# Performance work log

Hardware: AMD Instinct MI355X
Metric: run time of the kernel (lower is better)

Reference implementation:

```python
import jax, jax.numpy as jnp
import numpy as np

N, E, D, H, B = 10000, 160000, 128, 1, 4
SLOPE = 0.01  # negative_slope from DeepQNet default


def gat_layer(x, node_state, src, dst, W, att_src, att_dst, Wns, bns, bias):
    # x: [N,D] or [B,N,D]; node_state: [B,N,1]
    xs = x + node_state @ Wns + bns              # [B,N,D]
    Bx, Nn = xs.shape[0], xs.shape[1]
    h = (xs @ W).reshape(Bx, Nn, H, D)           # [B,N,H,C]
    a_src = (h * att_src).sum(-1)                # [B,N,H]
    a_dst = (h * att_dst).sum(-1)                # [B,N,H]
    ae = a_src[:, src] + a_dst[:, dst]           # [B,Etot,H]
    ae = jnp.where(ae > 0, ae, SLOPE * ae)       # leaky_relu
    ae_t = jnp.moveaxis(ae, 1, 0)                # [Etot,B,H]
    m = jax.ops.segment_max(ae_t, dst, num_segments=Nn)   # [N,B,H]
    e = jnp.exp(ae_t - m[dst])
    s = jax.ops.segment_sum(e, dst, num_segments=Nn)
    alpha = e / s[dst]                           # [Etot,B,H]
    h_e = jnp.moveaxis(h, 1, 0)                  # [N,B,H,C]
    msg = alpha[..., None] * h_e[src]            # [Etot,B,H,C]
    out = jax.ops.segment_sum(msg, dst, num_segments=Nn)  # [N,B,H,C]
    out = jnp.moveaxis(out, 0, 1).mean(2) + bias # concat=False -> head mean
    return jax.nn.relu(out)


def setup_inputs() -> dict:
    key = jax.random.key(0)
    ks = jax.random.split(key, 16)
    edges = jax.random.randint(ks[0], (2, E), 0, N)
    loop = jnp.arange(N)
    edge_index = jnp.concatenate([edges, jnp.stack([loop, loop])], axis=1)  # add_self_loops
    state = jax.random.uniform(ks[1], (B, N), dtype=jnp.float32)
    strucEmb = jax.random.normal(ks[2], (N, D), dtype=jnp.float32) * 0.1
    s = 0.05
    return {
        "state": state,
        "strucEmb": strucEmb,
        "edge_index": edge_index,
        "gat_W": jax.random.normal(ks[3], (3, D, H * D), dtype=jnp.float32) * s,
        "gat_att_src": jax.random.normal(ks[4], (3, H, D), dtype=jnp.float32) * s,
        "gat_att_dst": jax.random.normal(ks[5], (3, H, D), dtype=jnp.float32) * s,
        "gat_Wns": jax.random.normal(ks[6], (3, 1, D), dtype=jnp.float32) * s,
        "gat_bns": jnp.zeros((3, D), jnp.float32),
        "gat_bias": jnp.zeros((3, D), jnp.float32),
        "W1": jax.random.normal(ks[7], (D, D), dtype=jnp.float32) * s,
        "b1": jnp.zeros((D,), jnp.float32),
        "W2": jax.random.normal(ks[8], (D, D), dtype=jnp.float32) * s,
        "b2": jnp.zeros((D,), jnp.float32),
        "W3": jax.random.normal(ks[9], (2 * D, 1), dtype=jnp.float32) * s,
        "b3": jnp.zeros((1,), jnp.float32),
    }


def reference(state, strucEmb, edge_index, gat_W, gat_att_src, gat_att_dst,
              gat_Wns, gat_bns, gat_bias, W1, b1, W2, b2, W3, b3):
    src, dst = edge_index[0], edge_index[1]
    rs = state.reshape(state.shape[0], N, 1)     # [B,N,1]
    x = strucEmb
    for l in range(3):
        x = gat_layer(x, rs, src, dst, gat_W[l], gat_att_src[l], gat_att_dst[l],
                      gat_Wns[l], gat_bns[l], gat_bias[l])
    state_emb = x.sum(1)                         # [B,D]
    beta_state = state_emb @ W1 + b1             # [B,D]
    beta_action = x @ W2 + b2                    # [B,N,D]  (is_for_learn=True path)
    expand_state = jnp.broadcast_to(beta_state[:, None, :], beta_action.shape)
    out = jax.nn.relu(jnp.concatenate([expand_state, beta_action], axis=2))
    return out @ W3 + b3                         # [B,N,1]
```

## Files before the change

kernel.cpp:

```cpp
#include <hip/hip_runtime.h>
#include <math.h>

#define N_NODES 10000
#define B_SZ 4
#define SLOPE 0.01f
#define BN (B_SZ * N_NODES)
#define PADK 136

typedef __attribute__((ext_vector_type(8))) short short8;
typedef __attribute__((ext_vector_type(4))) float float4v;

__device__ __forceinline__ unsigned short f2bf(float f) {
    unsigned u = __builtin_bit_cast(unsigned, f);
    u += 0x7fffu + ((u >> 16) & 1u);
    return (unsigned short)(u >> 16);
}
__device__ __forceinline__ float bf2f(unsigned short s) {
    unsigned u = ((unsigned)s) << 16;
    return __builtin_bit_cast(float, u);
}
__device__ __forceinline__ float bflo(unsigned u) { return __builtin_bit_cast(float, u << 16); }
__device__ __forceinline__ float bfhi(unsigned u) { return __builtin_bit_cast(float, u & 0xffff0000u); }



__global__ __launch_bounds__(256) void setup_kernel(
    const float* __restrict__ strucEmb, const float* __restrict__ state,
    const float* __restrict__ Wns0, const float* __restrict__ bns0,
    const float* __restrict__ gatW, const float* __restrict__ W2,
    unsigned short* __restrict__ XS,
    unsigned short* __restrict__ whi, unsigned short* __restrict__ wlo,
    int* deg, int* cursor, float* state_emb)
{
    int bx = blockIdx.x, tid = threadIdx.x;
    if (bx < 2500) {
        int base = (bx * 256 + tid) * 8;
        int g = base >> 7, d0 = base & 127;
        int n = g - (g / N_NODES) * N_NODES;
        float st = state[g];
        const float* se = strucEmb + (size_t)n * 128 + d0;
        const float* wp = Wns0 + d0;
        const float* bp = bns0 + d0;
        short8 v;
#pragma unroll
        for (int j = 0; j < 8; j++)
            v[j] = (short)f2bf(se[j] + st * wp[j] + bp[j]);
        *(short8*)(XS + base) = v;
    } else if (bx < 2756) {
        int i = (bx - 2500) * 256 + tid;
        int w = i >> 14, rem = i & 16383;
        int k = rem >> 7, c = rem & 127;
        const float* src = (w < 3) ? (gatW + (size_t)w * 16384) : W2;
        float v = src[k * 128 + c];
        unsigned short h = f2bf(v);
        whi[w * 16384 + c * 128 + k] = h;
        wlo[w * 16384 + c * 128 + k] = f2bf(v - bf2f(h));
    } else {
        int i = (bx - 2756) * 256 + tid;
        if (i < N_NODES) { deg[i] = 0; cursor[i] = 0; }
        if (i < 512) state_emb[i] = 0.f;
    }
}


__global__ __launch_bounds__(256) void hist_kernel(const int* __restrict__ dst, int Etot, int* deg) {
    int e = blockIdx.x * 256 + threadIdx.x;
    if (e < Etot) atomicAdd(&deg[dst[e]], 1);
}

__global__ __launch_bounds__(1024) void scan_kernel(const int* __restrict__ deg, int* __restrict__ rowOff) {
    __shared__ int wsum[16];
    int tid = threadIdx.x;
    int lane = tid & 63, wid = tid >> 6;
    int base = tid * 10;
    int v[10]; int tot = 0;
#pragma unroll
    for (int j = 0; j < 10; j++) {
        int idx = base + j;
        int d = (idx < N_NODES) ? deg[idx] : 0;
        tot += d; v[j] = tot;
    }
    int incl = tot;
    for (int off = 1; off < 64; off <<= 1) {
        int t = __shfl_up(incl, off, 64);
        if (lane >= off) incl += t;
    }
    if (lane == 63) wsum[wid] = incl;
    __syncthreads();
    if (wid == 0) {
        int wv = (lane < 16) ? wsum[lane] : 0;
        for (int off = 1; off < 16; off <<= 1) {
            int t = __shfl_up(wv, off, 64);
            if (lane >= off) wv += t;
        }
        if (lane < 16) wsum[lane] = wv;
    }
    __syncthreads();
    int waveoff = (wid > 0) ? wsum[wid - 1] : 0;
    int excl = waveoff + incl - tot;
    if (tid == 0) rowOff[0] = 0;
#pragma unroll
    for (int j = 0; j < 10; j++) {
        int idx = base + j;
        if (idx < N_NODES) rowOff[idx + 1] = excl + v[j];
    }
}

__global__ __launch_bounds__(256) void scatter_kernel(const int* __restrict__ src, const int* __restrict__ dst,
                                                      int Etot, const int* __restrict__ rowOff,
                                                      int* cursor, int* __restrict__ srcLst) {
    int e = blockIdx.x * 256 + threadIdx.x;
    if (e < Etot) {
        int d = dst[e];
        int pos = rowOff[d] + atomicAdd(&cursor[d], 1);
        srcLst[pos] = src[e];
    }
}


__global__ __launch_bounds__(256) void gemm_att_mfma(
    const unsigned short* __restrict__ XS,
    const unsigned short* __restrict__ WThi, const unsigned short* __restrict__ WTlo,
    const float* __restrict__ attS, const float* __restrict__ attD,
    unsigned short* __restrict__ Hout, float* __restrict__ aSrcP, float* __restrict__ aDstP)
{
    __shared__ __align__(16) unsigned short sCus[64 * PADK];
    __shared__ float sAs[128], sAd[128];
    __shared__ float sPart[64 * 8];

    int tid = threadIdx.x;
    int g0 = blockIdx.x * 64;
    int w = tid >> 6, lane = tid & 63;
    int quad = lane >> 4, mcol = lane & 15;

    if (tid < 128) { sAs[tid] = attS[tid]; sAd[tid] = attD[tid]; }

    float4v acc[4][2];
#pragma unroll
    for (int mt = 0; mt < 4; mt++)
#pragma unroll
        for (int nt = 0; nt < 2; nt++) acc[mt][nt] = (float4v){0.f, 0.f, 0.f, 0.f};

#pragma unroll 1
    for (int term = 0; term < 2; term++) {
        const unsigned short* WT = term ? WTlo : WThi;
        short8 Bf[4][2];
#pragma unroll
        for (int kc = 0; kc < 4; kc++)
#pragma unroll
            for (int nt = 0; nt < 2; nt++)
                Bf[kc][nt] = *(const short8*)(WT + (w * 32 + nt * 16 + mcol) * 128 + kc * 32 + quad * 8);
#pragma unroll
        for (int kc = 0; kc < 4; kc++) {
            short8 Aa[4];
#pragma unroll
            for (int mt = 0; mt < 4; mt++)
                Aa[mt] = *(const short8*)(XS + (size_t)(g0 + mt * 16 + mcol) * 128 + kc * 32 + quad * 8);
#pragma unroll
            for (int mt = 0; mt < 4; mt++)
#pragma unroll
                for (int nt = 0; nt < 2; nt++)
                    acc[mt][nt] = __builtin_amdgcn_mfma_f32_16x16x32_bf16(Aa[mt], Bf[kc][nt], acc[mt][nt], 0, 0, 0);
        }
    }

    __syncthreads();

    float pp[16], pd[16];
#pragma unroll
    for (int r16 = 0; r16 < 16; r16++) { pp[r16] = 0.f; pd[r16] = 0.f; }
#pragma unroll
    for (int mt = 0; mt < 4; mt++)
#pragma unroll
        for (int nt = 0; nt < 2; nt++)
#pragma unroll
            for (int reg = 0; reg < 4; reg++) {
                int row = mt * 16 + quad * 4 + reg;
                int col = w * 32 + nt * 16 + mcol;
                float v = acc[mt][nt][reg];
                sCus[row * PADK + col] = f2bf(v);
                pp[mt * 4 + reg] += v * sAs[col];
                pd[mt * 4 + reg] += v * sAd[col];
            }
#pragma unroll
    for (int off = 1; off < 16; off <<= 1)
#pragma unroll
        for (int r16 = 0; r16 < 16; r16++) {
            pp[r16] += __shfl_xor(pp[r16], off);
            pd[r16] += __shfl_xor(pd[r16], off);
        }
    if (mcol == 0) {
#pragma unroll
        for (int r16 = 0; r16 < 16; r16++) {
            int row = (r16 >> 2) * 16 + quad * 4 + (r16 & 3);
            sPart[row * 8 + w * 2 + 0] = pp[r16];
            sPart[row * 8 + w * 2 + 1] = pd[r16];
        }
    }
    __syncthreads();

    for (int i = tid; i < 64 * 16; i += 256) {
        int r = i >> 4, c8 = i & 15;
        uint4 u = *(uint4*)(sCus + r * PADK + c8 * 8);
        *(uint4*)(Hout + (size_t)(g0 + r) * 128 + c8 * 8) = u;
    }
    if (tid < 64) {
        float s0 = sPart[tid * 8] + sPart[tid * 8 + 2] + sPart[tid * 8 + 4] + sPart[tid * 8 + 6];
        float s1 = sPart[tid * 8 + 1] + sPart[tid * 8 + 3] + sPart[tid * 8 + 5] + sPart[tid * 8 + 7];
        aSrcP[g0 + tid] = s0;
        aDstP[g0 + tid] = s1;
    }
}


__global__ __launch_bounds__(256) void sm_agg_kernel(
    const int* __restrict__ rowOff, const int* __restrict__ srcLst,
    const float* __restrict__ aSrcP, const float* __restrict__ aDstP,
    const unsigned short* __restrict__ H,
    const float* __restrict__ bias,
    const float* __restrict__ state, const float* __restrict__ wnsN,
    const float* __restrict__ bnsN, int addNext,
    unsigned short* __restrict__ Xout)
{
    __shared__ int   sSrcB[4 * 64];
    __shared__ float sAeB[4 * 64];
    int tid = threadIdx.x;
    int w = tid >> 6, t = tid & 63;
    int blk = blockIdx.x;
    int xcd = blk & 7;
    int b = xcd >> 1;
    int n = (((xcd & 1) * (N_NODES / 8) + (blk >> 3)) << 2) + w;
    int gb = b * N_NODES;
    int start = rowOff[n], end = rowOff[n + 1];
    int cnt = end - start;
    float adst = aDstP[gb + n];
    int*   sSrc = sSrcB + w * 64;
    float* sAe  = sAeB + w * 64;
    const uint4* H4 = (const uint4*)H;

    if (cnt <= 64) {
        float ae = -1e30f;
        if (t < cnt) {
            int sn = srcLst[start + t];
            sSrc[t] = sn;
            float v = aSrcP[gb + sn] + adst;
            ae = v > 0.f ? v : SLOPE * v;
        }
        float m = ae;
        m = fmaxf(m, __shfl_xor(m, 1));  m = fmaxf(m, __shfl_xor(m, 2));
        m = fmaxf(m, __shfl_xor(m, 4));  m = fmaxf(m, __shfl_xor(m, 8));
        m = fmaxf(m, __shfl_xor(m, 16)); m = fmaxf(m, __shfl_xor(m, 32));
        float e = (t < cnt) ? __expf(ae - m) : 0.f;
        float s = e;
        s += __shfl_xor(s, 1);  s += __shfl_xor(s, 2);  s += __shfl_xor(s, 4);
        s += __shfl_xor(s, 8);  s += __shfl_xor(s, 16); s += __shfl_xor(s, 32);
        float inv = 1.f / s;
        if (t < cnt) sAe[t] = e * inv;
        int cntE = (cnt + 3) & ~3;
        if (t >= cnt && t < cntE) { sSrc[t] = n; sAe[t] = 0.f; }

        int esub = t >> 4, c16 = t & 15;
        float a0 = 0.f, a1 = 0.f, a2 = 0.f, a3 = 0.f, a4 = 0.f, a5 = 0.f, a6 = 0.f, a7 = 0.f;
        int j = 0;
        for (; j + 16 <= cntE; j += 16) {
            uint4 h[4]; float al[4];
#pragma unroll
            for (int r = 0; r < 4; r++) {
                int jj = j + r * 4 + esub;
                h[r] = H4[(size_t)(gb + sSrc[jj]) * 16 + c16];
                al[r] = sAe[jj];
            }
#pragma unroll
            for (int r = 0; r < 4; r++) {
                a0 += al[r] * bflo(h[r].x); a1 += al[r] * bfhi(h[r].x);
                a2 += al[r] * bflo(h[r].y); a3 += al[r] * bfhi(h[r].y);
                a4 += al[r] * bflo(h[r].z); a5 += al[r] * bfhi(h[r].z);
                a6 += al[r] * bflo(h[r].w); a7 += al[r] * bfhi(h[r].w);
            }
        }
        for (; j < cntE; j += 4) {
            int jj = j + esub;
            uint4 hv = H4[(size_t)(gb + sSrc[jj]) * 16 + c16];
            float al = sAe[jj];
            a0 += al * bflo(hv.x); a1 += al * bfhi(hv.x);
            a2 += al * bflo(hv.y); a3 += al * bfhi(hv.y);
            a4 += al * bflo(hv.z); a5 += al * bfhi(hv.z);
            a6 += al * bflo(hv.w); a7 += al * bfhi(hv.w);
        }
        a0 += __shfl_xor(a0, 16); a1 += __shfl_xor(a1, 16);
        a2 += __shfl_xor(a2, 16); a3 += __shfl_xor(a3, 16);
        a4 += __shfl_xor(a4, 16); a5 += __shfl_xor(a5, 16);
        a6 += __shfl_xor(a6, 16); a7 += __shfl_xor(a7, 16);
        a0 += __shfl_xor(a0, 32); a1 += __shfl_xor(a1, 32);
        a2 += __shfl_xor(a2, 32); a3 += __shfl_xor(a3, 32);
        a4 += __shfl_xor(a4, 32); a5 += __shfl_xor(a5, 32);
        a6 += __shfl_xor(a6, 32); a7 += __shfl_xor(a7, 32);
        if (esub == 0) {
            int d0 = c16 * 8;
            float o0 = fmaxf(a0 + bias[d0],     0.f);
            float o1 = fmaxf(a1 + bias[d0 + 1], 0.f);
            float o2 = fmaxf(a2 + bias[d0 + 2], 0.f);
            float o3 = fmaxf(a3 + bias[d0 + 3], 0.f);
            float o4 = fmaxf(a4 + bias[d0 + 4], 0.f);
            float o5 = fmaxf(a5 + bias[d0 + 5], 0.f);
            float o6 = fmaxf(a6 + bias[d0 + 6], 0.f);
            float o7 = fmaxf(a7 + bias[d0 + 7], 0.f);
            if (addNext) {
                float st = state[gb + n];
                o0 += st * wnsN[d0]     + bnsN[d0];
                o1 += st * wnsN[d0 + 1] + bnsN[d0 + 1];
                o2 += st * wnsN[d0 + 2] + bnsN[d0 + 2];
                o3 += st * wnsN[d0 + 3] + bnsN[d0 + 3];
                o4 += st * wnsN[d0 + 4] + bnsN[d0 + 4];
                o5 += st * wnsN[d0 + 5] + bnsN[d0 + 5];
                o6 += st * wnsN[d0 + 6] + bnsN[d0 + 6];
                o7 += st * wnsN[d0 + 7] + bnsN[d0 + 7];
            }
            uint4 u;
            u.x = (unsigned)f2bf(o0) | ((unsigned)f2bf(o1) << 16);
            u.y = (unsigned)f2bf(o2) | ((unsigned)f2bf(o3) << 16);
            u.z = (unsigned)f2bf(o4) | ((unsigned)f2bf(o5) << 16);
            u.w = (unsigned)f2bf(o6) | ((unsigned)f2bf(o7) << 16);
            ((uint4*)Xout)[(size_t)(gb + n) * 16 + c16] = u;
        }
    } else {
        const unsigned* Hu = (const unsigned*)H;
        float m = -1e30f;
        for (int i = start + t; i < end; i += 64) {
            int sn = srcLst[i];
            float v = aSrcP[gb + sn] + adst;
            m = fmaxf(m, v > 0.f ? v : SLOPE * v);
        }
        m = fmaxf(m, __shfl_xor(m, 1));  m = fmaxf(m, __shfl_xor(m, 2));
        m = fmaxf(m, __shfl_xor(m, 4));  m = fmaxf(m, __shfl_xor(m, 8));
        m = fmaxf(m, __shfl_xor(m, 16)); m = fmaxf(m, __shfl_xor(m, 32));
        float s = 0.f;
        for (int i = start + t; i < end; i += 64) {
            int sn = srcLst[i];
            float v = aSrcP[gb + sn] + adst;
            float ae2 = v > 0.f ? v : SLOPE * v;
            s += __expf(ae2 - m);
        }
        s += __shfl_xor(s, 1);  s += __shfl_xor(s, 2);  s += __shfl_xor(s, 4);
        s += __shfl_xor(s, 8);  s += __shfl_xor(s, 16); s += __shfl_xor(s, 32);
        float inv = 1.f / s;
        float accx = 0.f, accy = 0.f;
        for (int c0 = start; c0 < end; c0 += 64) {
            int c = min(64, end - c0);
            if (t < c) {
                int sn = srcLst[c0 + t];
                sSrc[t] = sn;
                float v = aSrcP[gb + sn] + adst;
                float ae2 = v > 0.f ? v : SLOPE * v;
                sAe[t] = __expf(ae2 - m);
            }
            for (int j = 0; j < c; j++) {
                float a0 = sAe[j];
                unsigned h0 = Hu[(size_t)(gb + sSrc[j]) * 64 + t];
                accx += a0 * bflo(h0);
                accy += a0 * bfhi(h0);
            }
        }
        float ox = fmaxf(accx * inv + bias[2 * t], 0.f);
        float oy = fmaxf(accy * inv + bias[2 * t + 1], 0.f);
        if (addNext) {
            float st = state[gb + n];
            ox += st * wnsN[2 * t]     + bnsN[2 * t];
            oy += st * wnsN[2 * t + 1] + bnsN[2 * t + 1];
        }
        ((unsigned*)Xout)[(size_t)(gb + n) * 64 + t] =
            (unsigned)f2bf(ox) | ((unsigned)f2bf(oy) << 16);
    }
}


__global__ __launch_bounds__(128) void sum_nodes_kernel(const unsigned short* __restrict__ X, float* state_emb) {
    int cx = blockIdx.x, b = blockIdx.y, d = threadIdx.x;
    int n0 = cx * 157, n1 = n0 + 157;
    if (n1 > N_NODES) n1 = N_NODES;
    float acc = 0.f;
    for (int n = n0; n < n1; n++) acc += bf2f(X[(size_t)(b * N_NODES + n) * 128 + d]);
    atomicAdd(&state_emb[b * 128 + d], acc);
}


__global__ __launch_bounds__(256) void final_mfma(
    const unsigned short* __restrict__ X,
    const unsigned short* __restrict__ WThi, const unsigned short* __restrict__ WTlo,
    const float* __restrict__ b2, const float* __restrict__ W3,
    const float* __restrict__ b3,
    const float* __restrict__ state_emb, const float* __restrict__ W1,
    const float* __restrict__ b1,
    float* __restrict__ out)
{
    __shared__ float sB2[128], sW3[128];
    __shared__ float sPart[64 * 4];
    __shared__ float sC1p[8], sC1[4];

    int tid = threadIdx.x;
    int g0 = blockIdx.x * 64;
    int w = tid >> 6, lane = tid & 63;
    int quad = lane >> 4, mcol = lane & 15;

    if (tid < 128) { sB2[tid] = b2[tid]; sW3[tid] = W3[128 + tid]; }

    {
        int d = tid & 127;
        int bh = tid >> 7;
        float p0 = b1[d], p1 = b1[d];
        for (int k = 0; k < 128; k++) {
            float wv = W1[k * 128 + d];
            p0 += state_emb[bh * 128 + k] * wv;
            p1 += state_emb[(bh + 2) * 128 + k] * wv;
        }
        float w3d = W3[d];
        p0 = fmaxf(p0, 0.f) * w3d;
        p1 = fmaxf(p1, 0.f) * w3d;
#pragma unroll
        for (int off = 1; off < 64; off <<= 1) {
            p0 += __shfl_xor(p0, off);
            p1 += __shfl_xor(p1, off);
        }
        if (lane == 0) { sC1p[w * 2 + 0] = p0; sC1p[w * 2 + 1] = p1; }
    }
    __syncthreads();
    if (tid == 0) {
        sC1[0] = sC1p[0] + sC1p[2];  sC1[2] = sC1p[1] + sC1p[3];
        sC1[1] = sC1p[4] + sC1p[6];  sC1[3] = sC1p[5] + sC1p[7];
    }

    float4v acc[4][2];
#pragma unroll
    for (int mt = 0; mt < 4; mt++)
#pragma unroll
        for (int nt = 0; nt < 2; nt++) acc[mt][nt] = (float4v){0.f, 0.f, 0.f, 0.f};

#pragma unroll 1
    for (int term = 0; term < 2; term++) {
        const unsigned short* WT = term ? WTlo : WThi;
        short8 Bf[4][2];
#pragma unroll
        for (int kc = 0; kc < 4; kc++)
#pragma unroll
            for (int nt = 0; nt < 2; nt++)
                Bf[kc][nt] = *(const short8*)(WT + (w * 32 + nt * 16 + mcol) * 128 + kc * 32 + quad * 8);
#pragma unroll
        for (int kc = 0; kc < 4; kc++) {
            short8 Aa[4];
#pragma unroll
            for (int mt = 0; mt < 4; mt++)
                Aa[mt] = *(const short8*)(X + (size_t)(g0 + mt * 16 + mcol) * 128 + kc * 32 + quad * 8);
#pragma unroll
            for (int mt = 0; mt < 4; mt++)
#pragma unroll
                for (int nt = 0; nt < 2; nt++)
                    acc[mt][nt] = __builtin_amdgcn_mfma_f32_16x16x32_bf16(Aa[mt], Bf[kc][nt], acc[mt][nt], 0, 0, 0);
        }
    }

    float pp[16];
#pragma unroll
    for (int r16 = 0; r16 < 16; r16++) pp[r16] = 0.f;
#pragma unroll
    for (int mt = 0; mt < 4; mt++)
#pragma unroll
        for (int nt = 0; nt < 2; nt++)
#pragma unroll
            for (int reg = 0; reg < 4; reg++) {
                int col = w * 32 + nt * 16 + mcol;
                float v = acc[mt][nt][reg] + sB2[col];
                v = v > 0.f ? v : 0.f;
                pp[mt * 4 + reg] += v * sW3[col];
            }
#pragma unroll
    for (int off = 1; off < 16; off <<= 1)
#pragma unroll
        for (int r16 = 0; r16 < 16; r16++)
            pp[r16] += __shfl_xor(pp[r16], off);
    if (mcol == 0) {
#pragma unroll
        for (int r16 = 0; r16 < 16; r16++) {
            int row = (r16 >> 2) * 16 + quad * 4 + (r16 & 3);
            sPart[row * 4 + w] = pp[r16];
        }
    }
    __syncthreads();
    if (tid < 64) {
        float p = sPart[tid * 4] + sPart[tid * 4 + 1] + sPart[tid * 4 + 2] + sPart[tid * 4 + 3];
        int g = g0 + tid;
        int b = g / N_NODES;
        out[g] = p + sC1[b] + b3[0];
    }
}


extern "C" void kernel_launch(void* const* d_in, const int* in_sizes, int n_in,
                              void* d_out, int out_size, void* d_ws, size_t ws_size,
                              hipStream_t stream) {
    const float* state    = (const float*)d_in[0];
    const float* strucEmb = (const float*)d_in[1];
    const int*   edge_idx = (const int*)d_in[2];
    const float* gat_W    = (const float*)d_in[3];
    const float* gat_aS   = (const float*)d_in[4];
    const float* gat_aD   = (const float*)d_in[5];
    const float* gat_Wns  = (const float*)d_in[6];
    const float* gat_bns  = (const float*)d_in[7];
    const float* gat_bias = (const float*)d_in[8];
    const float* W1 = (const float*)d_in[9];
    const float* b1 = (const float*)d_in[10];
    const float* W2 = (const float*)d_in[11];
    const float* b2 = (const float*)d_in[12];
    const float* W3 = (const float*)d_in[13];
    const float* b3 = (const float*)d_in[14];
    float* out = (float*)d_out;

    int Etot = in_sizes[2] / 2;
    const int* srcArr = edge_idx;
    const int* dstArr = edge_idx + Etot;

    float* ws = (float*)d_ws;
    unsigned short* Xb = (unsigned short*)ws;
    unsigned short* Hb = (unsigned short*)(ws + 2560000);
    float* aSrcP       = ws + 5120000;
    float* aDstP       = ws + 5160000;
    float* state_emb   = ws + 5200000;
    unsigned short* whi = (unsigned short*)(ws + 5200516);
    unsigned short* wlo = whi + 4 * 16384;
    int*   iws         = (int*)(ws + 5200516 + 65536);
    int*   rowOff      = iws;
    int*   deg         = iws + 10001;
    int*   cursor      = deg + 10000;
    int*   srcLst      = cursor + 10000;

    setup_kernel<<<2796, 256, 0, stream>>>(strucEmb, state, gat_Wns, gat_bns,
                                           gat_W, W2, Xb, whi, wlo, deg, cursor, state_emb);
    hist_kernel<<<(Etot + 255) / 256, 256, 0, stream>>>(dstArr, Etot, deg);
    scan_kernel<<<1, 1024, 0, stream>>>(deg, rowOff);
    scatter_kernel<<<(Etot + 255) / 256, 256, 0, stream>>>(srcArr, dstArr, Etot, rowOff, cursor, srcLst);

    for (int l = 0; l < 3; l++) {
        gemm_att_mfma<<<BN / 64, 256, 0, stream>>>(
            Xb, whi + (size_t)l * 16384, wlo + (size_t)l * 16384,
            gat_aS + l * 128, gat_aD + l * 128, Hb, aSrcP, aDstP);
        sm_agg_kernel<<<N_NODES, 256, 0, stream>>>(
            rowOff, srcLst, aSrcP, aDstP, Hb, gat_bias + l * 128,
            state, gat_Wns + (l + 1 < 3 ? (l + 1) * 128 : 0),
            gat_bns + (l + 1 < 3 ? (l + 1) * 128 : 0), (l < 2) ? 1 : 0, Xb);
    }

    sum_nodes_kernel<<<dim3(64, B_SZ), 128, 0, stream>>>(Xb, state_emb);
    final_mfma<<<BN / 64, 256, 0, stream>>>(Xb, whi + 3 * 16384, wlo + 3 * 16384,
                                            b2, W3, b3, state_emb, W1, b1, out);
}
```

Before: 323.4 us.

## Process all four batches per wavefront in softmax-aggregation kernel

Each wavefront now handles one destination node across all four batch entries instead of one (node, batch) pair. CSR row offsets, source indices and shared-memory staging are loaded once and reused for four batches, and four independent H gathers are issued per edge. The grid shrinks fourfold and the XCD-aware block remapping is dropped. In exchange register pressure rises (32 accumulators plus in-flight loads), which may lower occupancy.

```diff
diff --git a/kernel.cpp b/kernel.cpp
--- a/kernel.cpp
+++ b/kernel.cpp
@@ -223,153 +223,196 @@
     unsigned short* __restrict__ Xout)
 {
     __shared__ int   sSrcB[4 * 64];
-    __shared__ float sAeB[4 * 64];
+    __shared__ float sAeB[4 * 4 * 64];
     int tid = threadIdx.x;
     int w = tid >> 6, t = tid & 63;
-    int blk = blockIdx.x;
-    int xcd = blk & 7;
-    int b = xcd >> 1;
-    int n = (((xcd & 1) * (N_NODES / 8) + (blk >> 3)) << 2) + w;
-    int gb = b * N_NODES;
+    int n = blockIdx.x * 4 + w;
     int start = rowOff[n], end = rowOff[n + 1];
     int cnt = end - start;
-    float adst = aDstP[gb + n];
     int*   sSrc = sSrcB + w * 64;
-    float* sAe  = sAeB + w * 64;
+    float* sAe  = sAeB + w * 256;
     const uint4* H4 = (const uint4*)H;
 
+    float adstb[4];
+#pragma unroll
+    for (int b = 0; b < 4; b++) adstb[b] = aDstP[b * N_NODES + n];
+
     if (cnt <= 64) {
-        float ae = -1e30f;
+        int sn = n;
+        if (t < cnt) { sn = srcLst[start + t]; sSrc[t] = sn; }
+        float ae0 = -1e30f, ae1 = -1e30f, ae2 = -1e30f, ae3 = -1e30f;
+        {
+            float v0 = aSrcP[0 * N_NODES + sn] + adstb[0];
+            float v1 = aSrcP[1 * N_NODES + sn] + adstb[1];
+            float v2 = aSrcP[2 * N_NODES + sn] + adstb[2];
+            float v3 = aSrcP[3 * N_NODES + sn] + adstb[3];
+            if (t < cnt) {
+                ae0 = v0 > 0.f ? v0 : SLOPE * v0;
+                ae1 = v1 > 0.f ? v1 : SLOPE * v1;
+                ae2 = v2 > 0.f ? v2 : SLOPE * v2;
+                ae3 = v3 > 0.f ? v3 : SLOPE * v3;
+            }
+        }
+        float m0 = ae0, m1 = ae1, m2 = ae2, m3 = ae3;
+#pragma unroll
+        for (int off = 1; off < 64; off <<= 1) {
+            m0 = fmaxf(m0, __shfl_xor(m0, off));
+            m1 = fmaxf(m1, __shfl_xor(m1, off));
+            m2 = fmaxf(m2, __shfl_xor(m2, off));
+            m3 = fmaxf(m3, __shfl_xor(m3, off));
+        }
+        float e0 = (t < cnt) ? __expf(ae0 - m0) : 0.f;
+        float e1 = (t < cnt) ? __expf(ae1 - m1) : 0.f;
+        float e2 = (t < cnt) ? __expf(ae2 - m2) : 0.f;
+        float e3 = (t < cnt) ? __expf(ae3 - m3) : 0.f;
+        float s0 = e0, s1 = e1, s2 = e2, s3 = e3;
+#pragma unroll
+        for (int off = 1; off < 64; off <<= 1) {
+            s0 += __shfl_xor(s0, off);
+            s1 += __shfl_xor(s1, off);
+            s2 += __shfl_xor(s2, off);
+            s3 += __shfl_xor(s3, off);
+        }
         if (t < cnt) {
-            int sn = srcLst[start + t];
-            sSrc[t] = sn;
-            float v = aSrcP[gb + sn] + adst;
-            ae = v > 0.f ? v : SLOPE * v;
-        }
-        float m = ae;
-        m = fmaxf(m, __shfl_xor(m, 1));  m = fmaxf(m, __shfl_xor(m, 2));
-        m = fmaxf(m, __shfl_xor(m, 4));  m = fmaxf(m, __shfl_xor(m, 8));
-        m = fmaxf(m, __shfl_xor(m, 16)); m = fmaxf(m, __shfl_xor(m, 32));
-        float e = (t < cnt) ? __expf(ae - m) : 0.f;
-        float s = e;
-        s += __shfl_xor(s, 1);  s += __shfl_xor(s, 2);  s += __shfl_xor(s, 4);
-        s += __shfl_xor(s, 8);  s += __shfl_xor(s, 16); s += __shfl_xor(s, 32);
-        float inv = 1.f / s;
-        if (t < cnt) sAe[t] = e * inv;
+            sAe[0 * 64 + t] = e0 / s0;
+            sAe[1 * 64 + t] = e1 / s1;
+            sAe[2 * 64 + t] = e2 / s2;
+            sAe[3 * 64 + t] = e3 / s3;
+        }
         int cntE = (cnt + 3) & ~3;
-        if (t >= cnt && t < cntE) { sSrc[t] = n; sAe[t] = 0.f; }
+        if (t >= cnt && t < cntE) {
+            sSrc[t] = n;
+            sAe[0 * 64 + t] = 0.f; sAe[1 * 64 + t] = 0.f;
+            sAe[2 * 64 + t] = 0.f; sAe[3 * 64 + t] = 0.f;
+        }
 
         int esub = t >> 4, c16 = t & 15;
-        float a0 = 0.f, a1 = 0.f, a2 = 0.f, a3 = 0.f, a4 = 0.f, a5 = 0.f, a6 = 0.f, a7 = 0.f;
+        float a[4][8];
+#pragma unroll
+        for (int b = 0; b < 4; b++)
+#pragma unroll
+            for (int k = 0; k < 8; k++) a[b][k] = 0.f;
+
         int j = 0;
-        for (; j + 16 <= cntE; j += 16) {
-            uint4 h[4]; float al[4];
-#pragma unroll
-            for (int r = 0; r < 4; r++) {
-                int jj = j + r * 4 + esub;
-                h[r] = H4[(size_t)(gb + sSrc[jj]) * 16 + c16];
-                al[r] = sAe[jj];
-            }
-#pragma unroll
-            for (int r = 0; r < 4; r++) {
-                a0 += al[r] * bflo(h[r].x); a1 += al[r] * bfhi(h[r].x);
-                a2 += al[r] * bflo(h[r].y); a3 += al[r] * bfhi(h[r].y);
-                a4 += al[r] * bflo(h[r].z); a5 += al[r] * bfhi(h[r].z);
-                a6 += al[r] * bflo(h[r].w); a7 += al[r] * bfhi(h[r].w);
+        for (; j + 8 <= cntE; j += 8) {
+            int j0 = j + esub, j1 = j + 4 + esub;
+            int sn0 = sSrc[j0], sn1 = sSrc[j1];
+            uint4 h0[4], h1[4]; float l0[4], l1[4];
+#pragma unroll
+            for (int b = 0; b < 4; b++) {
+                h0[b] = H4[((size_t)(b * N_NODES + sn0)) * 16 + c16];
+                h1[b] = H4[((size_t)(b * N_NODES + sn1)) * 16 + c16];
+                l0[b] = sAe[b * 64 + j0];
+                l1[b] = sAe[b * 64 + j1];
+            }
+#pragma unroll
+            for (int b = 0; b < 4; b++) {
+                a[b][0] += l0[b] * bflo(h0[b].x); a[b][1] += l0[b] * bfhi(h0[b].x);
+                a[b][2] += l0[b] * bflo(h0[b].y); a[b][3] += l0[b] * bfhi(h0[b].y);
+                a[b][4] += l0[b] * bflo(h0[b].z); a[b][5] += l0[b] * bfhi(h0[b].z);
+                a[b][6] += l0[b] * bflo(h0[b].w); a[b][7] += l0[b] * bfhi(h0[b].w);
+                a[b][0] += l1[b] * bflo(h1[b].x); a[b][1] += l1[b] * bfhi(h1[b].x);
+                a[b][2] += l1[b] * bflo(h1[b].y); a[b][3] += l1[b] * bfhi(h1[b].y);
+                a[b][4] += l1[b] * bflo(h1[b].z); a[b][5] += l1[b] * bfhi(h1[b].z);
+                a[b][6] += l1[b] * bflo(h1[b].w); a[b][7] += l1[b] * bfhi(h1[b].w);
             }
         }
         for (; j < cntE; j += 4) {
             int jj = j + esub;
-            uint4 hv = H4[(size_t)(gb + sSrc[jj]) * 16 + c16];
-            float al = sAe[jj];
-            a0 += al * bflo(hv.x); a1 += al * bfhi(hv.x);
-            a2 += al * bflo(hv.y); a3 += al * bfhi(hv.y);
-            a4 += al * bflo(hv.z); a5 += al * bfhi(hv.z);
-            a6 += al * bflo(hv.w); a7 += al * bfhi(hv.w);
-        }
-        a0 += __shfl_xor(a0, 16); a1 += __shfl_xor(a1, 16);
-        a2 += __shfl_xor(a2, 16); a3 += __shfl_xor(a3, 16);
-        a4 += __shfl_xor(a4, 16); a5 += __shfl_xor(a5, 16);
-        a6 += __shfl_xor(a6, 16); a7 += __shfl_xor(a7, 16);
-        a0 += __shfl_xor(a0, 32); a1 += __shfl_xor(a1, 32);
-        a2 += __shfl_xor(a2, 32); a3 += __shfl_xor(a3, 32);
-        a4 += __shfl_xor(a4, 32); a5 += __shfl_xor(a5, 32);
-        a6 += __shfl_xor(a6, 32); a7 += __shfl_xor(a7, 32);
+            int sn2 = sSrc[jj];
+            uint4 h[4]; float al[4];
+#pragma unroll
+            for (int b = 0; b < 4; b++) {
+                h[b] = H4[((size_t)(b * N_NODES + sn2)) * 16 + c16];
+                al[b] = sAe[b * 64 + jj];
+            }
+#pragma unroll
+            for (int b = 0; b < 4; b++) {
+                a[b][0] += al[b] * bflo(h[b].x); a[b][1] += al[b] * bfhi(h[b].x);
+                a[b][2] += al[b] * bflo(h[b].y); a[b][3] += al[b] * bfhi(h[b].y);
+                a[b][4] += al[b] * bflo(h[b].z); a[b][5] += al[b] * bfhi(h[b].z);
+                a[b][6] += al[b] * bflo(h[b].w); a[b][7] += al[b] * bfhi(h[b].w);
+            }
+        }
+#pragma unroll
+        for (int b = 0; b < 4; b++)
+#pragma unroll
+            for (int k = 0; k < 8; k++) {
+                a[b][k] += __shfl_xor(a[b][k], 16);
+                a[b][k] += __shfl_xor(a[b][k], 32);
+            }
         if (esub == 0) {
             int d0 = c16 * 8;
-            float o0 = fmaxf(a0 + bias[d0],     0.f);
-            float o1 = fmaxf(a1 + bias[d0 + 1], 0.f);
-            float o2 = fmaxf(a2 + bias[d0 + 2], 0.f);
-            float o3 = fmaxf(a3 + bias[d0 + 3], 0.f);
-            float o4 = fmaxf(a4 + bias[d0 + 4], 0.f);
-            float o5 = fmaxf(a5 + bias[d0 + 5], 0.f);
-            float o6 = fmaxf(a6 + bias[d0 + 6], 0.f);
-            float o7 = fmaxf(a7 + bias[d0 + 7], 0.f);
+#pragma unroll
+            for (int b = 0; b < 4; b++) {
+                float o[8];
+#pragma unroll
+                for (int k = 0; k < 8; k++) o[k] = fmaxf(a[b][k] + bias[d0 + k], 0.f);
+                if (addNext) {
+                    float st = state[b * N_NODES + n];
+#pragma unroll
+                    for (int k = 0; k < 8; k++) o[k] += st * wnsN[d0 + k] + bnsN[d0 + k];
+                }
+                uint4 u;
+                u.x = (unsigned)f2bf(o[0]) | ((unsigned)f2bf(o[1]) << 16);
+                u.y = (unsigned)f2bf(o[2]) | ((unsigned)f2bf(o[3]) << 16);
+                u.z = (unsigned)f2bf(o[4]) | ((unsigned)f2bf(o[5]) << 16);
+                u.w = (unsigned)f2bf(o[6]) | ((unsigned)f2bf(o[7]) << 16);
+                ((uint4*)Xout)[((size_t)(b * N_NODES + n)) * 16 + c16] = u;
+            }
+        }
+    } else {
+        const unsigned* Hu = (const unsigned*)H;
+#pragma unroll 1
+        for (int bb = 0; bb < 4; bb++) {
+            int gb = bb * N_NODES;
+            float adst = adstb[bb];
+            float m = -1e30f;
+            for (int i = start + t; i < end; i += 64) {
+                int sn = srcLst[i];
+                float v = aSrcP[gb + sn] + adst;
+                m = fmaxf(m, v > 0.f ? v : SLOPE * v);
+            }
+            m = fmaxf(m, __shfl_xor(m, 1));  m = fmaxf(m, __shfl_xor(m, 2));
+            m = fmaxf(m, __shfl_xor(m, 4));  m = fmaxf(m, __shfl_xor(m, 8));
+            m = fmaxf(m, __shfl_xor(m, 16)); m = fmaxf(m, __shfl_xor(m, 32));
+            float s = 0.f;
+            for (int i = start + t; i < end; i += 64) {
+                int sn = srcLst[i];
+                float v = aSrcP[gb + sn] + adst;
+                float ae2 = v > 0.f ? v : SLOPE * v;
+                s += __expf(ae2 - m);
+            }
+            s += __shfl_xor(s, 1);  s += __shfl_xor(s, 2);  s += __shfl_xor(s, 4);
+            s += __shfl_xor(s, 8);  s += __shfl_xor(s, 16); s += __shfl_xor(s, 32);
+            float inv = 1.f / s;
+            float accx = 0.f, accy = 0.f;
+            for (int c0 = start; c0 < end; c0 += 64) {
+                int c = min(64, end - c0);
+                if (t < c) {
+                    int sn = srcLst[c0 + t];
+                    sSrc[t] = sn;
+                    float v = aSrcP[gb + sn] + adst;
+                    float ae2 = v > 0.f ? v : SLOPE * v;
+                    sAe[t] = __expf(ae2 - m);
+                }
+                for (int j = 0; j < c; j++) {
+                    float a0 = sAe[j];
+                    unsigned h0 = Hu[(size_t)(gb + sSrc[j]) * 64 + t];
+                    accx += a0 * bflo(h0);
+                    accy += a0 * bfhi(h0);
+                }
+            }
+            float ox = fmaxf(accx * inv + bias[2 * t], 0.f);
+            float oy = fmaxf(accy * inv + bias[2 * t + 1], 0.f);
             if (addNext) {
                 float st = state[gb + n];
-                o0 += st * wnsN[d0]     + bnsN[d0];
-                o1 += st * wnsN[d0 + 1] + bnsN[d0 + 1];
-                o2 += st * wnsN[d0 + 2] + bnsN[d0 + 2];
-                o3 += st * wnsN[d0 + 3] + bnsN[d0 + 3];
-                o4 += st * wnsN[d0 + 4] + bnsN[d0 + 4];
-                o5 += st * wnsN[d0 + 5] + bnsN[d0 + 5];
-                o6 += st * wnsN[d0 + 6] + bnsN[d0 + 6];
-                o7 += st * wnsN[d0 + 7] + bnsN[d0 + 7];
-            }
-            uint4 u;
-            u.x = (unsigned)f2bf(o0) | ((unsigned)f2bf(o1) << 16);
-            u.y = (unsigned)f2bf(o2) | ((unsigned)f2bf(o3) << 16);
-            u.z = (unsigned)f2bf(o4) | ((unsigned)f2bf(o5) << 16);
-            u.w = (unsigned)f2bf(o6) | ((unsigned)f2bf(o7) << 16);
-            ((uint4*)Xout)[(size_t)(gb + n) * 16 + c16] = u;
-        }
-    } else {
-        const unsigned* Hu = (const unsigned*)H;
-        float m = -1e30f;
-        for (int i = start + t; i < end; i += 64) {
-            int sn = srcLst[i];
-            float v = aSrcP[gb + sn] + adst;
-            m = fmaxf(m, v > 0.f ? v : SLOPE * v);
-        }
-        m = fmaxf(m, __shfl_xor(m, 1));  m = fmaxf(m, __shfl_xor(m, 2));
-        m = fmaxf(m, __shfl_xor(m, 4));  m = fmaxf(m, __shfl_xor(m, 8));
-        m = fmaxf(m, __shfl_xor(m, 16)); m = fmaxf(m, __shfl_xor(m, 32));
-        float s = 0.f;
-        for (int i = start + t; i < end; i += 64) {
-            int sn = srcLst[i];
-            float v = aSrcP[gb + sn] + adst;
-            float ae2 = v > 0.f ? v : SLOPE * v;
-            s += __expf(ae2 - m);
-        }
-        s += __shfl_xor(s, 1);  s += __shfl_xor(s, 2);  s += __shfl_xor(s, 4);
-        s += __shfl_xor(s, 8);  s += __shfl_xor(s, 16); s += __shfl_xor(s, 32);
-        float inv = 1.f / s;
-        float accx = 0.f, accy = 0.f;
-        for (int c0 = start; c0 < end; c0 += 64) {
-            int c = min(64, end - c0);
-            if (t < c) {
-                int sn = srcLst[c0 + t];
-                sSrc[t] = sn;
-                float v = aSrcP[gb + sn] + adst;
-                float ae2 = v > 0.f ? v : SLOPE * v;
-                sAe[t] = __expf(ae2 - m);
-            }
-            for (int j = 0; j < c; j++) {
-                float a0 = sAe[j];
-                unsigned h0 = Hu[(size_t)(gb + sSrc[j]) * 64 + t];
-                accx += a0 * bflo(h0);
-                accy += a0 * bfhi(h0);
-            }
-        }
-        float ox = fmaxf(accx * inv + bias[2 * t], 0.f);
-        float oy = fmaxf(accy * inv + bias[2 * t + 1], 0.f);
-        if (addNext) {
-            float st = state[gb + n];
-            ox += st * wnsN[2 * t]     + bnsN[2 * t];
-            oy += st * wnsN[2 * t + 1] + bnsN[2 * t + 1];
-        }
-        ((unsigned*)Xout)[(size_t)(gb + n) * 64 + t] =
-            (unsigned)f2bf(ox) | ((unsigned)f2bf(oy) << 16);
+                ox += st * wnsN[2 * t]     + bnsN[2 * t];
+                oy += st * wnsN[2 * t + 1] + bnsN[2 * t + 1];
+            }
+            ((unsigned*)Xout)[(size_t)(gb + n) * 64 + t] =
+                (unsigned)f2bf(ox) | ((unsigned)f2bf(oy) << 16);
+        }
     }
 }
 
@@ -542,7 +585,7 @@
         gemm_att_mfma<<<BN / 64, 256, 0, stream>>>(
             Xb, whi + (size_t)l * 16384, wlo + (size_t)l * 16384,
             gat_aS + l * 128, gat_aD + l * 128, Hb, aSrcP, aDstP);
-        sm_agg_kernel<<<N_NODES, 256, 0, stream>>>(
+        sm_agg_kernel<<<N_NODES / 4, 256, 0, stream>>>(
             rowOff, srcLst, aSrcP, aDstP, Hb, gat_bias + l * 128,
             state, gat_Wns + (l + 1 < 3 ? (l + 1) * 128 : 0),
             gat_bns + (l + 1 < 3 ? (l + 1) * 128 : 0), (l < 2) ? 1 : 0, Xb);
```

Measured after the change: 349.9 us. 8.2% more time.
